# Performance work log

Measured on AMD Instinct MI355X. Metric: run time of the kernel, lower is better.

The kernel has to match this reference:

```python
import jax, jax.numpy as jnp
import numpy as np

B, T, D, H = 2, 2048, 2048, 16
HD = D // H  # 128


def setup_inputs() -> dict:
    key = jax.random.key(0)
    ks = jax.random.split(key, 9)
    s = 0.02
    return {
        "x": jax.random.normal(ks[0], (B, T, D), jnp.float32),
        "Wq": jax.random.normal(ks[1], (D, D), jnp.float32) * s,
        "bq": jnp.zeros((D,), jnp.float32),
        "Wk": jax.random.normal(ks[2], (D, HD), jnp.float32) * s,
        "bk": jnp.zeros((HD,), jnp.float32),
        "Wv": jax.random.normal(ks[3], (D, HD), jnp.float32) * s,
        "bv": jnp.zeros((HD,), jnp.float32),
        "Wo": jax.random.normal(ks[4], (D, D), jnp.float32) * s,
        "bo": jnp.zeros((D,), jnp.float32),
    }


def reference(x, Wq, bq, Wk, bk, Wv, bv, Wo, bo):
    Bx, Tx, Dx = x.shape
    hd = Wk.shape[1]
    h = Dx // hd
    # Q: (B, T, D) -> (B, H, T, hd)
    q = (x @ Wq + bq).reshape(Bx, Tx, h, hd).transpose(0, 2, 1, 3)
    # K, V: single shared head (B, T, hd) -> (B, 1, T, hd) via broadcast in einsum
    k = x @ Wk + bk  # (B, T, hd)
    v = x @ Wv + bv  # (B, T, hd)
    scale = 1.0 / jnp.sqrt(jnp.asarray(hd, x.dtype))
    # scores: (B, H, Tq, Tk); shared K broadcasts across all H query heads
    scores = jnp.einsum("bhqd,bkd->bhqk", q, k) * scale
    causal = jnp.tril(jnp.ones((Tx, Tx), bool))  # (Tq, Tk)
    scores = jnp.where(causal, scores, jnp.asarray(-1e9, scores.dtype))
    attn = jax.nn.softmax(scores, axis=-1)
    # out: (B, H, Tq, hd) with shared V
    out = jnp.einsum("bhqk,bkd->bhqd", attn, v)
    out = out.transpose(0, 2, 1, 3).reshape(Bx, Tx, Dx)
    return out @ Wo + bo
```

## Files before the change

### kernel.cpp

```cpp
#include <hip/hip_runtime.h>
#include <cstdint>
#include <cstddef>

#define Bq 2
#define Tq 2048
#define Dq 2048
#define Hq 16
#define HDq 128

using f32x4  = __attribute__((ext_vector_type(4))) float;
using short8 = __attribute__((ext_vector_type(8))) short;
typedef unsigned short ushort_t;

#define QSC 0.12751741772f

#define GLOAD_LDS16(gp, lp)                                                        \
  __builtin_amdgcn_global_load_lds((const __attribute__((address_space(1))) void*)(gp), \
                                   (__attribute__((address_space(3))) void*)(lp), 16, 0, 0)

__device__ inline ushort_t f2bf(float f) {
  uint32_t u = __float_as_uint(f);
  uint32_t r = (u + 0x7FFFu + ((u >> 16) & 1u)) >> 16;
  return (ushort_t)r;
}

__device__ inline uint32_t cvt_pk_bf16(float a, float b) {
  uint32_t r;
  asm("v_cvt_pk_bf16_f32 %0, %1, %2" : "=v"(r) : "v"(a), "v"(b));
  return r;
}

__global__ void cast_f32_bf16(const float* __restrict__ in, ushort_t* __restrict__ out, int n4) {
  int stride = gridDim.x * blockDim.x;
  for (int i = blockIdx.x * blockDim.x + threadIdx.x; i < n4; i += stride) {
    float4 v = reinterpret_cast<const float4*>(in)[i];
    ushort4 u;
    u.x = f2bf(v.x); u.y = f2bf(v.y); u.z = f2bf(v.z); u.w = f2bf(v.w);
    reinterpret_cast<ushort4*>(out)[i] = u;
  }
}

__global__ __launch_bounds__(512) void prep_weights(
    const float* __restrict__ Wq, const float* __restrict__ Wk,
    const float* __restrict__ Wv, const float* __restrict__ Wo,
    ushort_t* __restrict__ WqkvT, ushort_t* __restrict__ WoT) {
  const int z = blockIdx.z;
  const float* in;
  ushort_t* out;
  int C, row_off;
  if (z == 0)      { in = Wq; out = WqkvT; C = Dq;  row_off = 0; }
  else if (z == 1) { in = Wo; out = WoT;   C = Dq;  row_off = 0; }
  else if (z == 2) { in = Wk; out = WqkvT; C = HDq; row_off = 2048; }
  else             { in = Wv; out = WqkvT; C = HDq; row_off = 2176; }
  const int c0 = blockIdx.x * 64;
  if (c0 >= C) return;
  __shared__ float tile[64][65];
  const int r0 = blockIdx.y * 64;
  const int tx = threadIdx.x, ty = threadIdx.y;
#pragma unroll
  for (int i = ty; i < 64; i += 8)
    tile[i][tx] = in[(size_t)(r0 + i) * C + c0 + tx];
  __syncthreads();
#pragma unroll
  for (int i = ty; i < 64; i += 8)
    out[(size_t)(row_off + c0 + i) * Dq + r0 + tx] = f2bf(tile[tx][i]);
}

template <int OUT_MODE>
__global__ __launch_bounds__(256, 3) void gemm_bt(
    const ushort_t* __restrict__ A, const ushort_t* __restrict__ BT,
    const float* __restrict__ bias, void* __restrict__ Cout,
    int M, int N, int K, int NXT,
    ushort_t* __restrict__ Kout, ushort_t* __restrict__ VTout,
    const float* __restrict__ bias2, const float* __restrict__ bias3) {
  constexpr int BM = 128, BN = 128, BK = 64;
  __shared__ ushort_t As[BM * BK];
  __shared__ ushort_t Bs[BN * BK];
  const int tid = threadIdx.x;
  const int wave = tid >> 6, lane = tid & 63;
  const int wr = wave >> 1, wc = wave & 1;
  const int nwg = gridDim.x;
  const int orig = (blockIdx.x & 7) * (nwg >> 3) + (blockIdx.x >> 3);
  const int m0 = (orig / NXT) * BM, n0 = (orig % NXT) * BN;
  const int lrow = lane & 15;
  const int kswz0 = (((lane >> 4) ^ (lrow & 7)) << 3);
  const int kswz1 = (((4 + (lane >> 4)) ^ (lrow & 7)) << 3);

  int srcoff[4], dstoff[4];
#pragma unroll
  for (int p = 0; p < 4; ++p) {
    const int byteoff = p * 4096 + wave * 1024;
    const int e = (byteoff >> 1) + lane * 8;
    const int r = e >> 6, c = e & 63;
    const int cs = (((c >> 3) ^ (r & 7)) << 3);
    srcoff[p] = r * K + cs;
    dstoff[p] = byteoff;
  }

  f32x4 acc[4][4] = {};

  for (int k0 = 0; k0 < K; k0 += BK) {
#pragma unroll
    for (int p = 0; p < 4; ++p) {
      GLOAD_LDS16(A + (size_t)m0 * K + k0 + srcoff[p], (char*)As + dstoff[p]);
      GLOAD_LDS16(BT + (size_t)n0 * K + k0 + srcoff[p], (char*)Bs + dstoff[p]);
    }
    __syncthreads();
#pragma unroll
    for (int kk = 0; kk < 2; ++kk) {
      const int ksw = kk ? kswz1 : kswz0;
      short8 af[4], bfr[4];
#pragma unroll
      for (int i = 0; i < 4; ++i)
        af[i] = *(const short8*)&As[(wr * 64 + i * 16 + lrow) * BK + ksw];
#pragma unroll
      for (int i = 0; i < 4; ++i)
        bfr[i] = *(const short8*)&Bs[(wc * 64 + i * 16 + lrow) * BK + ksw];
#pragma unroll
      for (int mi = 0; mi < 4; ++mi)
#pragma unroll
        for (int ni = 0; ni < 4; ++ni)
          acc[mi][ni] = __builtin_amdgcn_mfma_f32_16x16x32_bf16(af[mi], bfr[ni], acc[mi][ni], 0, 0, 0);
    }
    __syncthreads();
  }

#pragma unroll
  for (int mi = 0; mi < 4; ++mi) {
#pragma unroll
    for (int ni = 0; ni < 4; ++ni) {
      int rbase = m0 + wr * 64 + mi * 16 + (lane >> 4) * 4;
      int col = n0 + wc * 64 + ni * 16 + lrow;
#pragma unroll
      for (int jj = 0; jj < 4; ++jj) {
        int r = rbase + jj;
        float v = acc[mi][ni][jj];
        if (OUT_MODE == 1) {
          ((float*)Cout)[(size_t)r * N + col] = v + bias[col];
        } else {
          if (col < Dq) {
            ((ushort_t*)Cout)[(size_t)r * Dq + col] = f2bf((v + bias[col]) * QSC);
          } else if (col < Dq + HDq) {
            int d = col - Dq;
            Kout[(size_t)r * HDq + d] = f2bf(v + bias2[d]);
          } else {
            int d = col - Dq - HDq;
            int b = r >> 11, t = r & (Tq - 1);
            VTout[((size_t)b * HDq + d) * Tq + t] = f2bf(v + bias3[d]);
          }
        }
      }
    }
  }
}

__global__ __launch_bounds__(256, 4) void mqa_attn(
    const ushort_t* __restrict__ Qb, const ushort_t* __restrict__ Kb,
    const ushort_t* __restrict__ VTb, ushort_t* __restrict__ Ab) {
  const int bid = blockIdx.x;
  const int jt = 31 - (bid >> 5);
  const int bh = bid & 31;
  const int b = bh >> 4, h = bh & 15;
  const int qrow0 = jt * 64;
  const int NT = jt + 1;

  const int wave = threadIdx.x >> 6, lane = threadIdx.x & 63;
  const int lrow = lane & 15, lk8 = (lane >> 4) * 8;
  const int rb = (lane >> 4) * 4;

  __shared__ ushort_t Ks[64 * 128];
  __shared__ ushort_t Vs[128 * 64];
  __shared__ ushort_t Pl[4][16 * 64];

  const size_t vtb = (size_t)b * HDq * Tq;
  const size_t kbb = (size_t)b * Tq * HDq;

  int kgoff[4], vgoff[4], lbase[4];
#pragma unroll
  for (int rnd = 0; rnd < 4; ++rnd) {
    const int base = rnd * 4096 + wave * 1024;
    const int L = base + lane * 16;
    const int r = L >> 8, c = L & 255;
    kgoff[rnd] = r * HDq + ((c ^ ((r & 7) << 4)) >> 1);
    const int r2 = L >> 7, c2 = L & 127;
    vgoff[rnd] = r2 * Tq + ((c2 ^ ((r2 & 7) << 4)) >> 1);
    lbase[rnd] = base;
  }

  auto stageK = [&](int kt) {
    const ushort_t* kp = Kb + kbb + (size_t)kt * 64 * HDq;
#pragma unroll
    for (int rnd = 0; rnd < 4; ++rnd)
      GLOAD_LDS16(kp + kgoff[rnd], (char*)Ks + lbase[rnd]);
  };
  auto stageV = [&](int kt) {
    const ushort_t* vp = VTb + vtb + kt * 64;
#pragma unroll
    for (int rnd = 0; rnd < 4; ++rnd)
      GLOAD_LDS16(vp + vgoff[rnd], (char*)Vs + lbase[rnd]);
  };

  short8 qf[4];
  {
    const size_t qrow = (size_t)(b * Tq + qrow0 + wave * 16 + lrow) * Dq + h * HDq;
#pragma unroll
    for (int dc = 0; dc < 4; ++dc)
      qf[dc] = *(const short8*)(Qb + qrow + dc * 32 + lk8);
  }

  f32x4 o[8] = {};
  float l_run[4] = {};

  stageK(0);
  stageV(0);
  __syncthreads();

  for (int s = 0; s < NT; ++s) {
    f32x4 sc[4] = {};
#pragma unroll
    for (int ni = 0; ni < 4; ++ni) {
      const int R = ni * 16 + lrow;
      short8 kf[4];
#pragma unroll
      for (int dc = 0; dc < 4; ++dc) {
        const int C = (dc * 64 + lk8 * 2) ^ ((R & 7) << 4);
        kf[dc] = *(const short8*)((const char*)Ks + R * 256 + C);
      }
#pragma unroll
      for (int dc = 0; dc < 4; ++dc)
        sc[ni] = __builtin_amdgcn_mfma_f32_16x16x32_bf16(qf[dc], kf[dc], sc[ni], 0, 0, 0);
    }

    __syncthreads();
    if (s + 1 < NT) stageK(s + 1);

    if (s == NT - 1) {
      const int qg = qrow0 + wave * 16 + rb;
#pragma unroll
      for (int ni = 0; ni < 4; ++ni) {
        const int kg = s * 64 + ni * 16 + lrow;
#pragma unroll
        for (int jj = 0; jj < 4; ++jj)
          if (kg > qg + jj) sc[ni][jj] = -1e30f;
      }
    }

#pragma unroll
    for (int ni = 0; ni < 4; ++ni) {
      float p0 = exp2f(fminf(sc[ni][0], 24.f) - 8.f);
      float p1 = exp2f(fminf(sc[ni][1], 24.f) - 8.f);
      float p2 = exp2f(fminf(sc[ni][2], 24.f) - 8.f);
      float p3 = exp2f(fminf(sc[ni][3], 24.f) - 8.f);
      l_run[0] += p0; l_run[1] += p1; l_run[2] += p2; l_run[3] += p3;
      const uint32_t u01 = cvt_pk_bf16(p0, p1);
      const uint32_t u23 = cvt_pk_bf16(p2, p3);
      const int col = ni * 16 + lrow;
      Pl[wave][(rb + 0) * 64 + (col ^ ((rb << 2) ^ 0))]  = (ushort_t)u01;
      Pl[wave][(rb + 1) * 64 + (col ^ ((rb << 2) ^ 8))]  = (ushort_t)(u01 >> 16);
      Pl[wave][(rb + 2) * 64 + (col ^ ((rb << 2) ^ 16))] = (ushort_t)u23;
      Pl[wave][(rb + 3) * 64 + (col ^ ((rb << 2) ^ 24))] = (ushort_t)(u23 >> 16);
    }

    short8 pa[2];
    const int fsw = ((lrow & 12) << 2) ^ ((lrow & 3) << 3);
#pragma unroll
    for (int kc = 0; kc < 2; ++kc)
      pa[kc] = *(const short8*)&Pl[wave][lrow * 64 + ((kc * 32 + lk8) ^ fsw)];
#pragma unroll
    for (int df = 0; df < 8; ++df) {
      const int R = df * 16 + lrow;
#pragma unroll
      for (int kc = 0; kc < 2; ++kc) {
        const int C = (kc * 64 + lk8 * 2) ^ ((R & 7) << 4);
        short8 vf = *(const short8*)((const char*)Vs + R * 128 + C);
        o[df] = __builtin_amdgcn_mfma_f32_16x16x32_bf16(pa[kc], vf, o[df], 0, 0, 0);
      }
    }

    __syncthreads();
    if (s + 1 < NT) stageV(s + 1);
  }

  float inv[4];
#pragma unroll
  for (int jj = 0; jj < 4; ++jj) {
    float l = l_run[jj];
#pragma unroll
    for (int off = 1; off < 16; off <<= 1) l += __shfl_xor(l, off, 64);
    inv[jj] = 1.f / l;
  }
  const size_t orow = (size_t)(b * Tq + qrow0 + wave * 16 + rb);
#pragma unroll
  for (int df = 0; df < 8; ++df) {
    const int col = h * HDq + df * 16 + lrow;
#pragma unroll
    for (int jj = 0; jj < 4; ++jj)
      Ab[(orow + jj) * Dq + col] = f2bf(o[df][jj] * inv[jj]);
  }
}

extern "C" void kernel_launch(void* const* d_in, const int* in_sizes, int n_in,
                              void* d_out, int out_size, void* d_ws, size_t ws_size,
                              hipStream_t stream) {
  const float* x  = (const float*)d_in[0];
  const float* Wq = (const float*)d_in[1];
  const float* bq = (const float*)d_in[2];
  const float* Wk = (const float*)d_in[3];
  const float* bk = (const float*)d_in[4];
  const float* Wv = (const float*)d_in[5];
  const float* bv = (const float*)d_in[6];
  const float* Wo = (const float*)d_in[7];
  const float* bo = (const float*)d_in[8];
  float* out = (float*)d_out;

  char* ws = (char*)d_ws;
  ushort_t* xb     = (ushort_t*)(ws);
  ushort_t* WqkvT  = (ushort_t*)(ws + 16777216);
  ushort_t* WoT    = (ushort_t*)(ws + 26214400);
  ushort_t* Qb     = (ushort_t*)(ws + 34603008);
  ushort_t* Kb     = (ushort_t*)(ws + 51380224);
  ushort_t* VTb    = (ushort_t*)(ws + 52428800);
  ushort_t* Ab     = (ushort_t*)(ws + 53477376);

  const int MT = Bq * Tq;

  cast_f32_bf16<<<2048, 256, 0, stream>>>(x, xb, MT * Dq / 4);
  prep_weights<<<dim3(32, 32, 4), dim3(64, 8), 0, stream>>>(Wq, Wk, Wv, Wo, WqkvT, WoT);

  gemm_bt<3><<<(2304 / 128) * (MT / 128), 256, 0, stream>>>(
      xb, WqkvT, bq, Qb, MT, 2304, Dq, 2304 / 128, Kb, VTb, bk, bv);

  mqa_attn<<<1024, 256, 0, stream>>>(Qb, Kb, VTb, Ab);

  gemm_bt<1><<<(Dq / 128) * (MT / 128), 256, 0, stream>>>(
      Ab, WoT, bo, out, MT, Dq, Dq, Dq / 128, nullptr, nullptr, nullptr, nullptr);
}
```

Measured before the change: 191.3 us.

## Share each K/V tile across two heads per block in MQA attention

Each attention block now handles two query heads: each wave covers 32 query rows of one head, using two 16-row MFMA fragments that share the K and V fragments read from LDS. This halves the grid and the number of K/V tile loads per head, raising MFMA work per LDS read. The block order also changes so the first 256 blocks take the longest causal tiles and the rest run in ascending order. The cost is more registers (launch bounds drop from 4 to 3 blocks per CU), a larger P buffer in LDS, and fewer blocks to balance the causal work across CUs.

```diff
diff --git a/kernel.cpp b/kernel.cpp
--- a/kernel.cpp
+++ b/kernel.cpp
@@ -154,23 +154,25 @@
   }
 }
 
-__global__ __launch_bounds__(256, 4) void mqa_attn(
+__global__ __launch_bounds__(256, 3) void mqa_attn(
     const ushort_t* __restrict__ Qb, const ushort_t* __restrict__ Kb,
     const ushort_t* __restrict__ VTb, ushort_t* __restrict__ Ab) {
   const int bid = blockIdx.x;
-  const int jt = 31 - (bid >> 5);
-  const int bh = bid & 31;
-  const int b = bh >> 4, h = bh & 15;
+  const int jt = (bid < 256) ? (31 - (bid >> 4)) : ((bid - 256) >> 4);
+  const int c = bid & 15;
+  const int b = c >> 3, hpp = c & 7;
   const int qrow0 = jt * 64;
   const int NT = jt + 1;
 
   const int wave = threadIdx.x >> 6, lane = threadIdx.x & 63;
   const int lrow = lane & 15, lk8 = (lane >> 4) * 8;
   const int rb = (lane >> 4) * 4;
+  const int h = hpp * 2 + (wave >> 1);
+  const int rhalf = (wave & 1) * 32;
 
   __shared__ ushort_t Ks[64 * 128];
   __shared__ ushort_t Vs[128 * 64];
-  __shared__ ushort_t Pl[4][16 * 64];
+  __shared__ ushort_t Pl[4][32 * 64];
 
   const size_t vtb = (size_t)b * HDq * Tq;
   const size_t kbb = (size_t)b * Tq * HDq;
@@ -180,8 +182,8 @@
   for (int rnd = 0; rnd < 4; ++rnd) {
     const int base = rnd * 4096 + wave * 1024;
     const int L = base + lane * 16;
-    const int r = L >> 8, c = L & 255;
-    kgoff[rnd] = r * HDq + ((c ^ ((r & 7) << 4)) >> 1);
+    const int r = L >> 8, cc = L & 255;
+    kgoff[rnd] = r * HDq + ((cc ^ ((r & 7) << 4)) >> 1);
     const int r2 = L >> 7, c2 = L & 127;
     vgoff[rnd] = r2 * Tq + ((c2 ^ ((r2 & 7) << 4)) >> 1);
     lbase[rnd] = base;
@@ -200,23 +202,24 @@
       GLOAD_LDS16(vp + vgoff[rnd], (char*)Vs + lbase[rnd]);
   };
 
-  short8 qf[4];
-  {
-    const size_t qrow = (size_t)(b * Tq + qrow0 + wave * 16 + lrow) * Dq + h * HDq;
+  short8 qf[2][4];
+#pragma unroll
+  for (int mi = 0; mi < 2; ++mi) {
+    const size_t qrow = (size_t)(b * Tq + qrow0 + rhalf + mi * 16 + lrow) * Dq + h * HDq;
 #pragma unroll
     for (int dc = 0; dc < 4; ++dc)
-      qf[dc] = *(const short8*)(Qb + qrow + dc * 32 + lk8);
-  }
-
-  f32x4 o[8] = {};
-  float l_run[4] = {};
+      qf[mi][dc] = *(const short8*)(Qb + qrow + dc * 32 + lk8);
+  }
+
+  f32x4 o[2][8] = {};
+  float l_run[2][4] = {};
 
   stageK(0);
   stageV(0);
   __syncthreads();
 
   for (int s = 0; s < NT; ++s) {
-    f32x4 sc[4] = {};
+    f32x4 sc[2][4] = {};
 #pragma unroll
     for (int ni = 0; ni < 4; ++ni) {
       const int R = ni * 16 + lrow;
@@ -227,45 +230,60 @@
         kf[dc] = *(const short8*)((const char*)Ks + R * 256 + C);
       }
 #pragma unroll
-      for (int dc = 0; dc < 4; ++dc)
-        sc[ni] = __builtin_amdgcn_mfma_f32_16x16x32_bf16(qf[dc], kf[dc], sc[ni], 0, 0, 0);
+      for (int dc = 0; dc < 4; ++dc) {
+        sc[0][ni] = __builtin_amdgcn_mfma_f32_16x16x32_bf16(qf[0][dc], kf[dc], sc[0][ni], 0, 0, 0);
+        sc[1][ni] = __builtin_amdgcn_mfma_f32_16x16x32_bf16(qf[1][dc], kf[dc], sc[1][ni], 0, 0, 0);
+      }
     }
 
     __syncthreads();
     if (s + 1 < NT) stageK(s + 1);
 
     if (s == NT - 1) {
-      const int qg = qrow0 + wave * 16 + rb;
+#pragma unroll
+      for (int mi = 0; mi < 2; ++mi) {
+        const int qr0 = qrow0 + rhalf + mi * 16;
+        if (s * 64 + 63 > qr0) {
+          const int qg = qr0 + rb;
+#pragma unroll
+          for (int ni = 0; ni < 4; ++ni) {
+            const int kg = s * 64 + ni * 16 + lrow;
+#pragma unroll
+            for (int jj = 0; jj < 4; ++jj)
+              if (kg > qg + jj) sc[mi][ni][jj] = -1e30f;
+          }
+        }
+      }
+    }
+
+#pragma unroll
+    for (int mi = 0; mi < 2; ++mi) {
 #pragma unroll
       for (int ni = 0; ni < 4; ++ni) {
-        const int kg = s * 64 + ni * 16 + lrow;
-#pragma unroll
-        for (int jj = 0; jj < 4; ++jj)
-          if (kg > qg + jj) sc[ni][jj] = -1e30f;
-      }
-    }
-
-#pragma unroll
-    for (int ni = 0; ni < 4; ++ni) {
-      float p0 = exp2f(fminf(sc[ni][0], 24.f) - 8.f);
-      float p1 = exp2f(fminf(sc[ni][1], 24.f) - 8.f);
-      float p2 = exp2f(fminf(sc[ni][2], 24.f) - 8.f);
-      float p3 = exp2f(fminf(sc[ni][3], 24.f) - 8.f);
-      l_run[0] += p0; l_run[1] += p1; l_run[2] += p2; l_run[3] += p3;
-      const uint32_t u01 = cvt_pk_bf16(p0, p1);
-      const uint32_t u23 = cvt_pk_bf16(p2, p3);
-      const int col = ni * 16 + lrow;
-      Pl[wave][(rb + 0) * 64 + (col ^ ((rb << 2) ^ 0))]  = (ushort_t)u01;
-      Pl[wave][(rb + 1) * 64 + (col ^ ((rb << 2) ^ 8))]  = (ushort_t)(u01 >> 16);
-      Pl[wave][(rb + 2) * 64 + (col ^ ((rb << 2) ^ 16))] = (ushort_t)u23;
-      Pl[wave][(rb + 3) * 64 + (col ^ ((rb << 2) ^ 24))] = (ushort_t)(u23 >> 16);
-    }
-
-    short8 pa[2];
+        float p0 = exp2f(fminf(sc[mi][ni][0], 24.f) - 8.f);
+        float p1 = exp2f(fminf(sc[mi][ni][1], 24.f) - 8.f);
+        float p2 = exp2f(fminf(sc[mi][ni][2], 24.f) - 8.f);
+        float p3 = exp2f(fminf(sc[mi][ni][3], 24.f) - 8.f);
+        l_run[mi][0] += p0; l_run[mi][1] += p1;
+        l_run[mi][2] += p2; l_run[mi][3] += p3;
+        const uint32_t u01 = cvt_pk_bf16(p0, p1);
+        const uint32_t u23 = cvt_pk_bf16(p2, p3);
+        const int col = ni * 16 + lrow;
+        const int rowb = mi * 16 + rb;
+        Pl[wave][(rowb + 0) * 64 + (col ^ ((rb << 2) ^ 0))]  = (ushort_t)u01;
+        Pl[wave][(rowb + 1) * 64 + (col ^ ((rb << 2) ^ 8))]  = (ushort_t)(u01 >> 16);
+        Pl[wave][(rowb + 2) * 64 + (col ^ ((rb << 2) ^ 16))] = (ushort_t)u23;
+        Pl[wave][(rowb + 3) * 64 + (col ^ ((rb << 2) ^ 24))] = (ushort_t)(u23 >> 16);
+      }
+    }
+
+    short8 pa[2][2];
     const int fsw = ((lrow & 12) << 2) ^ ((lrow & 3) << 3);
 #pragma unroll
-    for (int kc = 0; kc < 2; ++kc)
-      pa[kc] = *(const short8*)&Pl[wave][lrow * 64 + ((kc * 32 + lk8) ^ fsw)];
+    for (int mi = 0; mi < 2; ++mi)
+#pragma unroll
+      for (int kc = 0; kc < 2; ++kc)
+        pa[mi][kc] = *(const short8*)&Pl[wave][(mi * 16 + lrow) * 64 + ((kc * 32 + lk8) ^ fsw)];
 #pragma unroll
     for (int df = 0; df < 8; ++df) {
       const int R = df * 16 + lrow;
@@ -273,7 +291,8 @@
       for (int kc = 0; kc < 2; ++kc) {
         const int C = (kc * 64 + lk8 * 2) ^ ((R & 7) << 4);
         short8 vf = *(const short8*)((const char*)Vs + R * 128 + C);
-        o[df] = __builtin_amdgcn_mfma_f32_16x16x32_bf16(pa[kc], vf, o[df], 0, 0, 0);
+        o[0][df] = __builtin_amdgcn_mfma_f32_16x16x32_bf16(pa[0][kc], vf, o[0][df], 0, 0, 0);
+        o[1][df] = __builtin_amdgcn_mfma_f32_16x16x32_bf16(pa[1][kc], vf, o[1][df], 0, 0, 0);
       }
     }
 
@@ -281,21 +300,24 @@
     if (s + 1 < NT) stageV(s + 1);
   }
 
-  float inv[4];
-#pragma unroll
-  for (int jj = 0; jj < 4; ++jj) {
-    float l = l_run[jj];
-#pragma unroll
-    for (int off = 1; off < 16; off <<= 1) l += __shfl_xor(l, off, 64);
-    inv[jj] = 1.f / l;
-  }
-  const size_t orow = (size_t)(b * Tq + qrow0 + wave * 16 + rb);
-#pragma unroll
-  for (int df = 0; df < 8; ++df) {
-    const int col = h * HDq + df * 16 + lrow;
-#pragma unroll
-    for (int jj = 0; jj < 4; ++jj)
-      Ab[(orow + jj) * Dq + col] = f2bf(o[df][jj] * inv[jj]);
+#pragma unroll
+  for (int mi = 0; mi < 2; ++mi) {
+    float inv[4];
+#pragma unroll
+    for (int jj = 0; jj < 4; ++jj) {
+      float l = l_run[mi][jj];
+#pragma unroll
+      for (int off = 1; off < 16; off <<= 1) l += __shfl_xor(l, off, 64);
+      inv[jj] = 1.f / l;
+    }
+    const size_t orow = (size_t)(b * Tq + qrow0 + rhalf + mi * 16 + rb);
+#pragma unroll
+    for (int df = 0; df < 8; ++df) {
+      const int col = h * HDq + df * 16 + lrow;
+#pragma unroll
+      for (int jj = 0; jj < 4; ++jj)
+        Ab[(orow + jj) * Dq + col] = f2bf(o[mi][df][jj] * inv[jj]);
+    }
   }
 }
 
@@ -330,7 +352,7 @@
   gemm_bt<3><<<(2304 / 128) * (MT / 128), 256, 0, stream>>>(
       xb, WqkvT, bq, Qb, MT, 2304, Dq, 2304 / 128, Kb, VTb, bk, bv);
 
-  mqa_attn<<<1024, 256, 0, stream>>>(Qb, Kb, VTb, Ab);
+  mqa_attn<<<512, 256, 0, stream>>>(Qb, Kb, VTb, Ab);
 
   gemm_bt<1><<<(Dq / 128) * (MT / 128), 256, 0, stream>>>(
       Ab, WoT, bo, out, MT, Dq, Dq, Dq / 128, nullptr, nullptr, nullptr, nullptr);
```

Result: slower. 311.0 us (+62.6%).
